# Optimization experiments

Measured on AMD Instinct MI355X. Metric: run time of the kernel, lower is better.

## Reference

```python
import jax, jax.numpy as jnp
import numpy as np

NUM_HEAD = 8


def setup_inputs() -> dict:
    key = jax.random.key(0)
    ks = jax.random.split(key, 8)
    B, N, M, C, R = 4, 2048, 2048, 256, 128
    s = 1.0 / np.sqrt(C)
    return {
        "input_q": jax.random.normal(ks[0], (B, N, C), jnp.float32),
        "input_k": jax.random.normal(ks[1], (B, M, C), jnp.float32),
        "input_v": jax.random.normal(ks[2], (B, M, C), jnp.float32),
        "rpe_indices": jax.random.randint(ks[3], (B, N, M), 0, R, jnp.int32),
        "key_masks": jnp.zeros((B, M), jnp.float32),
        "Wq": jax.random.normal(ks[4], (C, C), jnp.float32) * s,
        "bq": jnp.zeros((C,), jnp.float32),
        "Wk": jax.random.normal(ks[5], (C, C), jnp.float32) * s,
        "bk": jnp.zeros((C,), jnp.float32),
        "Wv": jax.random.normal(ks[6], (C, C), jnp.float32) * s,
        "bv": jnp.zeros((C,), jnp.float32),
        "rpe_bank": jax.random.normal(ks[7], (R, C), jnp.float32),
    }


def reference(input_q, input_k, input_v, rpe_indices, key_masks,
              Wq, bq, Wk, bk, Wv, bv, rpe_bank):
    B, N, C = input_q.shape
    M = input_k.shape[1]
    H = NUM_HEAD
    Dh = C // H
    R = rpe_bank.shape[0]

    # projections -> (B, H, len, Dh)
    q = (input_q @ Wq + bq).reshape(B, N, H, Dh).transpose(0, 2, 1, 3)
    k = (input_k @ Wk + bk).reshape(B, M, H, Dh).transpose(0, 2, 1, 3)
    v = (input_v @ Wv + bv).reshape(B, M, H, Dh).transpose(0, 2, 1, 3)

    # RPE bank split per head: (H, R, Dh)
    rpe = rpe_bank.reshape(R, H, Dh).transpose(1, 0, 2)

    # q . rpe for all bins, then gather per (n, m) relative index
    scores_p_all = jnp.einsum('bhnd,hrd->bhnr', q, rpe)            # (B,H,N,R)
    idx = jnp.broadcast_to(rpe_indices[:, None, :, :], (B, H, N, M))
    scores_p = jnp.take_along_axis(scores_p_all, idx, axis=-1)     # (B,H,N,M)

    scores_e = jnp.einsum('bhnd,bhmd->bhnm', q, k)                 # (B,H,N,M)
    scores = (scores_e + scores_p) / jnp.sqrt(jnp.asarray(Dh, q.dtype))
    scores = scores + key_masks[:, None, None, :]

    attn = jax.nn.softmax(scores, axis=-1)
    out = jnp.einsum('bhnm,bhmd->bhnd', attn, v)                   # (B,H,N,Dh)
    return out.transpose(0, 2, 1, 3).reshape(B, N, C)
```

## Files before the change

kernel.cpp:

```cpp
#include <hip/hip_runtime.h>
#include <hip/hip_bf16.h>

#define B_ 4
#define N_ 2048
#define M_ 2048
#define C_ 256
#define H_ 8
#define DH_ 32
#define R_ 128

typedef __bf16 bf16x8 __attribute__((ext_vector_type(8)));
typedef float f32x4 __attribute__((ext_vector_type(4)));

#define QSCL 0.25503486f
#define LOG2E 1.4426950408889634f
#define DTHR 11.5f

__device__ __forceinline__ float fast_exp2(float x) {
    float r;
    asm("v_exp_f32 %0, %1" : "=v"(r) : "v"(x));
    return r;
}

#define GLOAD_LDS4(gp, lp)                                            \
    __builtin_amdgcn_global_load_lds(                                 \
        (const __attribute__((address_space(1))) void*)(gp),          \
        (__attribute__((address_space(3))) void*)(lp), 4, 0, 0)

__global__ __launch_bounds__(256) void wtrans_kernel(
    const float* __restrict__ Wq, const float* __restrict__ Wk,
    const float* __restrict__ Wv, __bf16* __restrict__ out)
{
    __shared__ float t[32][33];
    int pz = blockIdx.z;
    const float* W = pz == 0 ? Wq : (pz == 1 ? Wk : Wv);
    int j0 = blockIdx.x * 32, k0 = blockIdx.y * 32;
    int tx = threadIdx.x, ty = threadIdx.y;
#pragma unroll
    for (int i = 0; i < 4; ++i)
        t[ty + 8 * i][tx] = W[(k0 + ty + 8 * i) * C_ + j0 + tx];
    __syncthreads();
    __bf16* o = out + (size_t)pz * C_ * C_;
#pragma unroll
    for (int i = 0; i < 4; ++i)
        o[(j0 + ty + 8 * i) * C_ + k0 + tx] = (__bf16)t[tx][ty + 8 * i];
}

__global__ __launch_bounds__(256) void proj_kernel(
    const float* __restrict__ Xq, const float* __restrict__ Xk, const float* __restrict__ Xv,
    const float* __restrict__ bq, const float* __restrict__ bk, const float* __restrict__ bv,
    const __bf16* __restrict__ Wt,
    __bf16* __restrict__ qb, __bf16* __restrict__ kb, __bf16* __restrict__ vt)
{
    int pz = blockIdx.z;
    const float* X = pz == 0 ? Xq : (pz == 1 ? Xk : Xv);
    const float* bias = pz == 0 ? bq : (pz == 1 ? bk : bv);
    const __bf16* W = Wt + (size_t)pz * C_ * C_;

    int r0 = blockIdx.x * 64;
    int w = threadIdx.x >> 6, lane = threadIdx.x & 63;
    int lg = lane >> 4, lr = lane & 15;
    int rw = r0 + w * 16;

    f32x4 z = {0.f, 0.f, 0.f, 0.f};
    f32x4 acc[16];
#pragma unroll
    for (int ns = 0; ns < 16; ++ns) acc[ns] = z;

    for (int ks = 0; ks < 8; ++ks) {
        const float* ap = X + (size_t)(rw + lr) * C_ + ks * 32 + lg * 8;
        float4 a0 = *(const float4*)ap;
        float4 a1 = *(const float4*)(ap + 4);
        bf16x8 af;
        af[0] = (__bf16)a0.x; af[1] = (__bf16)a0.y; af[2] = (__bf16)a0.z; af[3] = (__bf16)a0.w;
        af[4] = (__bf16)a1.x; af[5] = (__bf16)a1.y; af[6] = (__bf16)a1.z; af[7] = (__bf16)a1.w;
        if (pz < 2) {
#pragma unroll
            for (int ns = 0; ns < 16; ++ns) {
                bf16x8 bfv = *(const bf16x8*)(W + (size_t)(ns * 16 + lr) * C_ + ks * 32 + lg * 8);
                acc[ns] = __builtin_amdgcn_mfma_f32_16x16x32_bf16(bfv, af, acc[ns], 0, 0, 0);
            }
        } else {
#pragma unroll
            for (int ns = 0; ns < 16; ++ns) {
                bf16x8 bfv = *(const bf16x8*)(W + (size_t)(ns * 16 + lr) * C_ + ks * 32 + lg * 8);
                acc[ns] = __builtin_amdgcn_mfma_f32_16x16x32_bf16(af, bfv, acc[ns], 0, 0, 0);
            }
        }
    }

    if (pz < 2) {
        int ng = rw + lr;
        int bb = ng >> 11, n = ng & (N_ - 1);
        unsigned short* dst = (unsigned short*)(pz == 0 ? qb : kb);
#pragma unroll
        for (int ns = 0; ns < 16; ++ns) {
            int j0b = ns * 16 + 4 * lg;
            float4 b4 = *(const float4*)(bias + j0b);
            int hh = j0b >> 5, d0 = j0b & 31;
            float v0 = acc[ns][0] + b4.x, v1 = acc[ns][1] + b4.y;
            float v2 = acc[ns][2] + b4.z, v3 = acc[ns][3] + b4.w;
            if (pz == 0) { v0 *= QSCL; v1 *= QSCL; v2 *= QSCL; v3 *= QSCL; }
            ushort4 pk;
            pk.x = __builtin_bit_cast(unsigned short, (__bf16)v0);
            pk.y = __builtin_bit_cast(unsigned short, (__bf16)v1);
            pk.z = __builtin_bit_cast(unsigned short, (__bf16)v2);
            pk.w = __builtin_bit_cast(unsigned short, (__bf16)v3);
            *(ushort4*)(dst + ((((size_t)bb * H_ + hh) * 2048 + n) * DH_ + d0)) = pk;
        }
    } else {
        int r = rw + lg * 4;
        int bb = r >> 11, n = r & (N_ - 1);
        int np = (n & ~31) | (((n >> 2) & 3) << 3) | (((n >> 4) & 1) << 2);
#pragma unroll
        for (int ns = 0; ns < 16; ++ns) {
            int j = ns * 16 + lr;
            float bj = bias[j];
            int hh = j >> 5, d = j & 31;
            ushort4 pk;
            pk.x = __builtin_bit_cast(unsigned short, (__bf16)(acc[ns][0] + bj));
            pk.y = __builtin_bit_cast(unsigned short, (__bf16)(acc[ns][1] + bj));
            pk.z = __builtin_bit_cast(unsigned short, (__bf16)(acc[ns][2] + bj));
            pk.w = __builtin_bit_cast(unsigned short, (__bf16)(acc[ns][3] + bj));
            *(ushort4*)((unsigned short*)vt + (((size_t)bb * H_ + hh) * DH_ + d) * M_ + np) = pk;
        }
    }
}

__global__ __launch_bounds__(512, 4) void attn_kernel(
    const __bf16* __restrict__ qb, const __bf16* __restrict__ kb,
    const __bf16* __restrict__ vt, const int* __restrict__ ridx,
    const float* __restrict__ kmask, const float* __restrict__ rbank,
    float* __restrict__ out)
{
    __shared__ __bf16 Pall[H_][16][R_];
    __shared__ int idxS[2][16 * 64];

    int lin = blockIdx.x;
    int b = (lin & 7) >> 1;
    int xq = ((lin >> 3) << 1) | (lin & 1);
    int n0 = xq * 16;

    int h = threadIdx.x >> 6, lane = threadIdx.x & 63;
    int lg = lane >> 4, lr = lane & 15;
    f32x4 z = {0.f, 0.f, 0.f, 0.f};

    const int* ixblk = ridx + ((size_t)b * N_ + n0) * M_;

#pragma unroll
    for (int i = 0; i < 2; ++i) {
        int r = 2 * h + i;
        int sw = 4 * (r & 7);
        GLOAD_LDS4(ixblk + (size_t)r * M_ + (lane ^ sw), &idxS[0][r * 64]);
    }

    bf16x8 qf = *(const bf16x8*)(qb + (((size_t)b * H_ + h) * N_ + n0 + lr) * DH_ + lg * 8);

    for (int rs = 0; rs < R_ / 16; ++rs) {
        const float* rp = rbank + (size_t)(rs * 16 + lr) * C_ + h * DH_ + lg * 8;
        float4 r0v = *(const float4*)rp;
        float4 r1v = *(const float4*)(rp + 4);
        bf16x8 rf;
        rf[0] = (__bf16)r0v.x; rf[1] = (__bf16)r0v.y; rf[2] = (__bf16)r0v.z; rf[3] = (__bf16)r0v.w;
        rf[4] = (__bf16)r1v.x; rf[5] = (__bf16)r1v.y; rf[6] = (__bf16)r1v.z; rf[7] = (__bf16)r1v.w;
        f32x4 pc = __builtin_amdgcn_mfma_f32_16x16x32_bf16(qf, rf, z, 0, 0, 0);
#pragma unroll
        for (int reg = 0; reg < 4; ++reg)
            Pall[h][lg * 4 + reg][rs * 16 + lr] = (__bf16)pc[reg];
    }

    const __bf16* Kh = kb + ((size_t)b * H_ + h) * M_ * DH_;
    const __bf16* Vh = vt + ((size_t)b * H_ + h) * DH_ * M_;
    const float* km = kmask + (size_t)b * M_;
    const __bf16* PallR = &Pall[h][lr][0];
    int swzR = 4 * (lr & 7);

    bf16x8 kf[4];
#pragma unroll
    for (int ms = 0; ms < 4; ++ms)
        kf[ms] = *(const bf16x8*)(Kh + (size_t)(ms * 16 + lr) * DH_ + lg * 8);

    __syncthreads();

    float mrow = -1e30f, lloc = 0.f;
    f32x4 acc[2] = {z, z};
    int cb = 0;

#pragma unroll 2
    for (int mt = 0; mt < M_ / 64; ++mt) {
        int m0 = mt * 64;
        int m0n = (mt < 31) ? m0 + 64 : m0;

#pragma unroll
        for (int i = 0; i < 2; ++i) {
            int r = 2 * h + i;
            int sw = 4 * (r & 7);
            GLOAD_LDS4(ixblk + (size_t)r * M_ + m0n + (lane ^ sw), &idxS[cb ^ 1][r * 64]);
        }

        bf16x8 kf_n[4];
#pragma unroll
        for (int ms = 0; ms < 4; ++ms)
            kf_n[ms] = *(const bf16x8*)(Kh + (size_t)(m0n + ms * 16 + lr) * DH_ + lg * 8);

        bf16x8 vf[4];
#pragma unroll
        for (int ds = 0; ds < 2; ++ds)
#pragma unroll
            for (int ks = 0; ks < 2; ++ks)
                vf[ds * 2 + ks] = *(const bf16x8*)(Vh + (size_t)(ds * 16 + lr) * M_ + m0 + ks * 32 + lg * 8);
        float4 mkv[4];
#pragma unroll
        for (int ms = 0; ms < 4; ++ms)
            mkv[ms] = *(const float4*)(km + m0 + ms * 16 + 4 * lg);

        int4 ixv[4];
#pragma unroll
        for (int ms = 0; ms < 4; ++ms)
            ixv[ms] = *(const int4*)&idxS[cb][lr * 64 + ((16 * ms + 4 * lg) ^ swzR)];
        float sv[16];
#pragma unroll
        for (int ms = 0; ms < 4; ++ms) {
            sv[ms * 4 + 0] = (float)PallR[ixv[ms].x];
            sv[ms * 4 + 1] = (float)PallR[ixv[ms].y];
            sv[ms * 4 + 2] = (float)PallR[ixv[ms].z];
            sv[ms * 4 + 3] = (float)PallR[ixv[ms].w];
        }

        f32x4 st[4];
#pragma unroll
        for (int ms = 0; ms < 4; ++ms)
            st[ms] = __builtin_amdgcn_mfma_f32_16x16x32_bf16(kf[ms], qf, z, 0, 0, 0);

#pragma unroll
        for (int ms = 0; ms < 4; ++ms) {
            sv[ms * 4 + 0] = fmaf(mkv[ms].x, LOG2E, st[ms][0] + sv[ms * 4 + 0]);
            sv[ms * 4 + 1] = fmaf(mkv[ms].y, LOG2E, st[ms][1] + sv[ms * 4 + 1]);
            sv[ms * 4 + 2] = fmaf(mkv[ms].z, LOG2E, st[ms][2] + sv[ms * 4 + 2]);
            sv[ms * 4 + 3] = fmaf(mkv[ms].w, LOG2E, st[ms][3] + sv[ms * 4 + 3]);
        }

        float t0 = fmaxf(fmaxf(sv[0], sv[1]), fmaxf(sv[2], sv[3]));
        float t1 = fmaxf(fmaxf(sv[4], sv[5]), fmaxf(sv[6], sv[7]));
        float t2 = fmaxf(fmaxf(sv[8], sv[9]), fmaxf(sv[10], sv[11]));
        float t3 = fmaxf(fmaxf(sv[12], sv[13]), fmaxf(sv[14], sv[15]));
        float pmax = fmaxf(fmaxf(t0, t1), fmaxf(t2, t3));

        if (!__all(pmax - mrow <= DTHR)) {
            float rmax = fmaxf(pmax, __shfl_xor(pmax, 16));
            rmax = fmaxf(rmax, __shfl_xor(rmax, 32));
            float mnew = fmaxf(mrow, rmax);
            float alpha = fast_exp2(mrow - mnew);
            mrow = mnew;
            lloc *= alpha;
#pragma unroll
            for (int reg = 0; reg < 4; ++reg) {
                float aB = __shfl(alpha, lg * 4 + reg);
                acc[0][reg] *= aB;
                acc[1][reg] *= aB;
            }
        }

        float pq[16];
#pragma unroll
        for (int j = 0; j < 16; ++j) pq[j] = fast_exp2(sv[j] - mrow);
        {
            float s0 = (pq[0] + pq[1]) + (pq[2] + pq[3]);
            float s1 = (pq[4] + pq[5]) + (pq[6] + pq[7]);
            float s2 = (pq[8] + pq[9]) + (pq[10] + pq[11]);
            float s3 = (pq[12] + pq[13]) + (pq[14] + pq[15]);
            lloc += (s0 + s1) + (s2 + s3);
        }

#pragma unroll
        for (int ks = 0; ks < 2; ++ks) {
            bf16x8 pf;
#pragma unroll
            for (int e = 0; e < 8; ++e) pf[e] = (__bf16)pq[8 * ks + e];
#pragma unroll
            for (int ds = 0; ds < 2; ++ds)
                acc[ds] = __builtin_amdgcn_mfma_f32_16x16x32_bf16(pf, vf[ds * 2 + ks], acc[ds], 0, 0, 0);
        }

        __syncthreads();
        cb ^= 1;
#pragma unroll
        for (int ms = 0; ms < 4; ++ms) kf[ms] = kf_n[ms];
    }

    float lrow = lloc + __shfl_xor(lloc, 16);
    lrow += __shfl_xor(lrow, 32);
#pragma unroll
    for (int reg = 0; reg < 4; ++reg) {
        float lB = __shfl(lrow, lg * 4 + reg);
        float inv = 1.0f / lB;
        size_t rb = ((size_t)b * N_ + n0 + lg * 4 + reg) * C_ + h * DH_;
        out[rb + lr] = acc[0][reg] * inv;
        out[rb + 16 + lr] = acc[1][reg] * inv;
    }
}

extern "C" void kernel_launch(void* const* d_in, const int* in_sizes, int n_in,
                              void* d_out, int out_size, void* d_ws, size_t ws_size,
                              hipStream_t stream) {
    const float* Xq = (const float*)d_in[0];
    const float* Xk = (const float*)d_in[1];
    const float* Xv = (const float*)d_in[2];
    const int* ridx = (const int*)d_in[3];
    const float* kmask = (const float*)d_in[4];
    const float* Wq = (const float*)d_in[5];
    const float* bq = (const float*)d_in[6];
    const float* Wk = (const float*)d_in[7];
    const float* bk = (const float*)d_in[8];
    const float* Wv = (const float*)d_in[9];
    const float* bv = (const float*)d_in[10];
    const float* rbank = (const float*)d_in[11];
    float* outp = (float*)d_out;

    char* ws = (char*)d_ws;
    __bf16* Wt = (__bf16*)ws;
    __bf16* qb = (__bf16*)(ws + 393216);
    __bf16* kb = (__bf16*)(ws + 393216 + 4194304);
    __bf16* vt = (__bf16*)(ws + 393216 + 8388608);

    wtrans_kernel<<<dim3(8, 8, 3), dim3(32, 8), 0, stream>>>(Wq, Wk, Wv, Wt);
    proj_kernel<<<dim3(128, 1, 3), 256, 0, stream>>>(Xq, Xk, Xv, bq, bk, bv, Wt, qb, kb, vt);
    attn_kernel<<<512, 512, 0, stream>>>(qb, kb, vt, ridx, kmask, rbank, outp);
}
```

Before: 171.7 us.

## Load RPE indices straight to registers with 2-deep prefetch, drop LDS staging

```diff
diff --git a/kernel.cpp b/kernel.cpp
--- a/kernel.cpp
+++ b/kernel.cpp
@@ -21,11 +21,6 @@
     asm("v_exp_f32 %0, %1" : "=v"(r) : "v"(x));
     return r;
 }
-
-#define GLOAD_LDS4(gp, lp)                                            \
-    __builtin_amdgcn_global_load_lds(                                 \
-        (const __attribute__((address_space(1))) void*)(gp),          \
-        (__attribute__((address_space(3))) void*)(lp), 4, 0, 0)
 
 __global__ __launch_bounds__(256) void wtrans_kernel(
     const float* __restrict__ Wq, const float* __restrict__ Wk,
@@ -133,8 +128,7 @@
     const float* __restrict__ kmask, const float* __restrict__ rbank,
     float* __restrict__ out)
 {
-    __shared__ __bf16 Pall[H_][16][R_];
-    __shared__ int idxS[2][16 * 64];
+    __shared__ __bf16 Pall[H_][16][130];
 
     int lin = blockIdx.x;
     int b = (lin & 7) >> 1;
@@ -145,14 +139,13 @@
     int lg = lane >> 4, lr = lane & 15;
     f32x4 z = {0.f, 0.f, 0.f, 0.f};
 
-    const int* ixblk = ridx + ((size_t)b * N_ + n0) * M_;
-
-#pragma unroll
-    for (int i = 0; i < 2; ++i) {
-        int r = 2 * h + i;
-        int sw = 4 * (r & 7);
-        GLOAD_LDS4(ixblk + (size_t)r * M_ + (lane ^ sw), &idxS[0][r * 64]);
-    }
+    const int* ixr = ridx + ((size_t)b * N_ + n0 + lr) * M_ + 4 * lg;
+
+    int4 ixc[4], ixn[4];
+#pragma unroll
+    for (int ms = 0; ms < 4; ++ms) ixc[ms] = *(const int4*)(ixr + 16 * ms);
+#pragma unroll
+    for (int ms = 0; ms < 4; ++ms) ixn[ms] = *(const int4*)(ixr + 64 + 16 * ms);
 
     bf16x8 qf = *(const bf16x8*)(qb + (((size_t)b * H_ + h) * N_ + n0 + lr) * DH_ + lg * 8);
 
@@ -173,31 +166,33 @@
     const __bf16* Vh = vt + ((size_t)b * H_ + h) * DH_ * M_;
     const float* km = kmask + (size_t)b * M_;
     const __bf16* PallR = &Pall[h][lr][0];
-    int swzR = 4 * (lr & 7);
 
     bf16x8 kf[4];
 #pragma unroll
     for (int ms = 0; ms < 4; ++ms)
         kf[ms] = *(const bf16x8*)(Kh + (size_t)(ms * 16 + lr) * DH_ + lg * 8);
 
-    __syncthreads();
-
     float mrow = -1e30f, lloc = 0.f;
     f32x4 acc[2] = {z, z};
-    int cb = 0;
 
 #pragma unroll 2
     for (int mt = 0; mt < M_ / 64; ++mt) {
         int m0 = mt * 64;
         int m0n = (mt < 31) ? m0 + 64 : m0;
-
-#pragma unroll
-        for (int i = 0; i < 2; ++i) {
-            int r = 2 * h + i;
-            int sw = 4 * (r & 7);
-            GLOAD_LDS4(ixblk + (size_t)r * M_ + m0n + (lane ^ sw), &idxS[cb ^ 1][r * 64]);
-        }
-
+        int m2 = (mt < 30) ? m0 + 128 : (M_ - 64);
+
+        float sv[16];
+#pragma unroll
+        for (int ms = 0; ms < 4; ++ms) {
+            sv[ms * 4 + 0] = (float)PallR[ixc[ms].x];
+            sv[ms * 4 + 1] = (float)PallR[ixc[ms].y];
+            sv[ms * 4 + 2] = (float)PallR[ixc[ms].z];
+            sv[ms * 4 + 3] = (float)PallR[ixc[ms].w];
+        }
+
+        int4 ix2[4];
+#pragma unroll
+        for (int ms = 0; ms < 4; ++ms) ix2[ms] = *(const int4*)(ixr + m2 + 16 * ms);
         bf16x8 kf_n[4];
 #pragma unroll
         for (int ms = 0; ms < 4; ++ms)
@@ -213,19 +208,6 @@
 #pragma unroll
         for (int ms = 0; ms < 4; ++ms)
             mkv[ms] = *(const float4*)(km + m0 + ms * 16 + 4 * lg);
-
-        int4 ixv[4];
-#pragma unroll
-        for (int ms = 0; ms < 4; ++ms)
-            ixv[ms] = *(const int4*)&idxS[cb][lr * 64 + ((16 * ms + 4 * lg) ^ swzR)];
-        float sv[16];
-#pragma unroll
-        for (int ms = 0; ms < 4; ++ms) {
-            sv[ms * 4 + 0] = (float)PallR[ixv[ms].x];
-            sv[ms * 4 + 1] = (float)PallR[ixv[ms].y];
-            sv[ms * 4 + 2] = (float)PallR[ixv[ms].z];
-            sv[ms * 4 + 3] = (float)PallR[ixv[ms].w];
-        }
 
         f32x4 st[4];
 #pragma unroll
@@ -282,10 +264,8 @@
                 acc[ds] = __builtin_amdgcn_mfma_f32_16x16x32_bf16(pf, vf[ds * 2 + ks], acc[ds], 0, 0, 0);
         }
 
-        __syncthreads();
-        cb ^= 1;
-#pragma unroll
-        for (int ms = 0; ms < 4; ++ms) kf[ms] = kf_n[ms];
+#pragma unroll
+        for (int ms = 0; ms < 4; ++ms) { ixc[ms] = ixn[ms]; ixn[ms] = ix2[ms]; kf[ms] = kf_n[ms]; }
     }
 
     float lrow = lloc + __shfl_xor(lloc, 16);
```

Result: slower. 220.4 us (+28.3%).

## Split attention over key dimension in two halves and merge partials

Applied to the files above, without the earlier changes.

```diff
diff --git a/kernel.cpp b/kernel.cpp
--- a/kernel.cpp
+++ b/kernel.cpp
@@ -131,21 +131,23 @@
     const __bf16* __restrict__ qb, const __bf16* __restrict__ kb,
     const __bf16* __restrict__ vt, const int* __restrict__ ridx,
     const float* __restrict__ kmask, const float* __restrict__ rbank,
-    float* __restrict__ out)
+    float* __restrict__ Opart, float* __restrict__ Ms, float* __restrict__ Ls)
 {
     __shared__ __bf16 Pall[H_][16][R_];
     __shared__ int idxS[2][16 * 64];
 
     int lin = blockIdx.x;
+    int mh = lin & 1;
     int b = (lin & 7) >> 1;
-    int xq = ((lin >> 3) << 1) | (lin & 1);
+    int xq = lin >> 3;
     int n0 = xq * 16;
+    int mbase = mh * (M_ / 2);
 
     int h = threadIdx.x >> 6, lane = threadIdx.x & 63;
     int lg = lane >> 4, lr = lane & 15;
     f32x4 z = {0.f, 0.f, 0.f, 0.f};
 
-    const int* ixblk = ridx + ((size_t)b * N_ + n0) * M_;
+    const int* ixblk = ridx + ((size_t)b * N_ + n0) * M_ + mbase;
 
 #pragma unroll
     for (int i = 0; i < 2; ++i) {
@@ -169,9 +171,9 @@
             Pall[h][lg * 4 + reg][rs * 16 + lr] = (__bf16)pc[reg];
     }
 
-    const __bf16* Kh = kb + ((size_t)b * H_ + h) * M_ * DH_;
-    const __bf16* Vh = vt + ((size_t)b * H_ + h) * DH_ * M_;
-    const float* km = kmask + (size_t)b * M_;
+    const __bf16* Kh = kb + ((size_t)b * H_ + h) * M_ * DH_ + (size_t)mbase * DH_;
+    const __bf16* Vh = vt + ((size_t)b * H_ + h) * DH_ * M_ + mbase;
+    const float* km = kmask + (size_t)b * M_ + mbase;
     const __bf16* PallR = &Pall[h][lr][0];
     int swzR = 4 * (lr & 7);
 
@@ -187,9 +189,9 @@
     int cb = 0;
 
 #pragma unroll 2
-    for (int mt = 0; mt < M_ / 64; ++mt) {
+    for (int mt = 0; mt < 16; ++mt) {
         int m0 = mt * 64;
-        int m0n = (mt < 31) ? m0 + 64 : m0;
+        int m0n = (mt < 15) ? m0 + 64 : m0;
 
 #pragma unroll
         for (int i = 0; i < 2; ++i) {
@@ -290,14 +292,49 @@
 
     float lrow = lloc + __shfl_xor(lloc, 16);
     lrow += __shfl_xor(lrow, 32);
+    float* Op = Opart + (((size_t)mh * B_ + b) * N_ + n0) * C_ + h * DH_;
 #pragma unroll
     for (int reg = 0; reg < 4; ++reg) {
-        float lB = __shfl(lrow, lg * 4 + reg);
-        float inv = 1.0f / lB;
-        size_t rb = ((size_t)b * N_ + n0 + lg * 4 + reg) * C_ + h * DH_;
-        out[rb + lr] = acc[0][reg] * inv;
-        out[rb + 16 + lr] = acc[1][reg] * inv;
-    }
+        size_t rb = (size_t)(4 * lg + reg) * C_;
+        Op[rb + lr] = acc[0][reg];
+        Op[rb + 16 + lr] = acc[1][reg];
+    }
+    if (lane < 16) {
+        size_t si = (((size_t)mh * B_ + b) * H_ + h) * N_ + n0 + lr;
+        Ms[si] = mrow;
+        Ls[si] = lrow;
+    }
+}
+
+__global__ __launch_bounds__(256) void merge_kernel(
+    const float* __restrict__ Opart, const float* __restrict__ Ms,
+    const float* __restrict__ Ls, float* __restrict__ out)
+{
+    int t = blockIdx.x * 256 + threadIdx.x;
+    int c4 = t & 63;
+    int n = (t >> 6) & (N_ - 1);
+    int bb = t >> 17;
+    int h = c4 >> 3;
+
+    size_t s0 = ((size_t)bb * H_ + h) * N_ + n;
+    size_t s1 = (((size_t)B_ + bb) * H_ + h) * N_ + n;
+    float m0 = Ms[s0], m1 = Ms[s1];
+    float l0 = Ls[s0], l1 = Ls[s1];
+    float mm = fmaxf(m0, m1);
+    float w0 = fast_exp2(m0 - mm), w1 = fast_exp2(m1 - mm);
+    float inv = 1.0f / (l0 * w0 + l1 * w1);
+    w0 *= inv; w1 *= inv;
+
+    size_t o0i = ((size_t)bb * N_ + n) * C_ + c4 * 4;
+    size_t o1i = (((size_t)B_ + bb) * N_ + n) * C_ + c4 * 4;
+    float4 o0 = *(const float4*)(Opart + o0i);
+    float4 o1 = *(const float4*)(Opart + o1i);
+    float4 r;
+    r.x = o0.x * w0 + o1.x * w1;
+    r.y = o0.y * w0 + o1.y * w1;
+    r.z = o0.z * w0 + o1.z * w1;
+    r.w = o0.w * w0 + o1.w * w1;
+    *(float4*)(out + ((size_t)bb * N_ + n) * C_ + c4 * 4) = r;
 }
 
 extern "C" void kernel_launch(void* const* d_in, const int* in_sizes, int n_in,
@@ -322,8 +359,12 @@
     __bf16* qb = (__bf16*)(ws + 393216);
     __bf16* kb = (__bf16*)(ws + 393216 + 4194304);
     __bf16* vt = (__bf16*)(ws + 393216 + 8388608);
+    float* Opart = (float*)(ws + 12976128);
+    float* Msb = (float*)(ws + 12976128 + 16777216);
+    float* Lsb = (float*)(ws + 12976128 + 16777216 + 524288);
 
     wtrans_kernel<<<dim3(8, 8, 3), dim3(32, 8), 0, stream>>>(Wq, Wk, Wv, Wt);
     proj_kernel<<<dim3(128, 1, 3), 256, 0, stream>>>(Xq, Xk, Xv, bq, bk, bv, Wt, qb, kb, vt);
-    attn_kernel<<<512, 512, 0, stream>>>(qb, kb, vt, ridx, kmask, rbank, outp);
-}
+    attn_kernel<<<1024, 512, 0, stream>>>(qb, kb, vt, ridx, kmask, rbank, Opart, Msb, Lsb);
+    merge_kernel<<<2048, 256, 0, stream>>>(Opart, Msb, Lsb, outp);
+}
```

Result: slower. 202.5 us (+17.9%).
